# Kernel tuning notes

Measured on AMD Instinct MI355X. Metric: run time of the kernel, lower is better.

## Reference

```python
import jax, jax.numpy as jnp
import numpy as np

B_, S, D_IN, D_OUT, R = 4, 2048, 2048, 2048, 16

def setup_inputs() -> dict:
    key = jax.random.key(0)
    k = jax.random.split(key, 5)
    x = jax.random.normal(k[0], (B_, S, D_IN), dtype=jnp.float32)
    W = jax.random.normal(k[1], (D_OUT, D_IN), dtype=jnp.float32) * (1.0 / np.sqrt(D_IN))
    b = jax.random.normal(k[2], (D_OUT,), dtype=jnp.float32) * 0.02
    A = jax.random.normal(k[3], (R, D_IN), dtype=jnp.float32) * 0.02  # nn.init.normal_(std=0.02)
    Bm = jax.random.normal(k[4], (D_OUT, R), dtype=jnp.float32) * 0.02
    scale = jnp.asarray(0.8, dtype=jnp.float32)
    return {"x": x, "W": W, "b": b, "A": A, "B": Bm, "scale": scale}

def reference(x, W, b, A, B, scale):
    # base linear: y = x @ W^T + b
    orig = jnp.einsum('bsd,od->bso', x, W) + b
    # LoRA: scale * (x @ A^T) @ B^T
    h = jnp.einsum('bsd,rd->bsr', x, A)          # [B,S,r]
    lora = jnp.einsum('bsr,or->bso', h, B) * scale
    return orig + lora
```

## Files before the change

### kernel.cpp

```cpp
#include <hip/hip_runtime.h>
#include <hip/hip_bf16.h>
#include <cstdint>


typedef __bf16 bf16x8 __attribute__((ext_vector_type(8)));
typedef float floatx4 __attribute__((ext_vector_type(4)));
typedef unsigned short ushort8 __attribute__((ext_vector_type(8)));

#define BM 256
#define BN 256
#define BK 64

__device__ __forceinline__ void gload_lds16(const void* g, void* l) {
    __builtin_amdgcn_global_load_lds((__attribute__((address_space(1))) void*)g,
                                     (__attribute__((address_space(3))) void*)l,
                                     16, 0, 0);
}

__device__ __forceinline__ unsigned short f2bf_bits(float f) {
    unsigned int u = __float_as_uint(f);
    u += 0x7FFFu + ((u >> 16) & 1u);
    return (unsigned short)(u >> 16);
}

__global__ __launch_bounds__(256)
void aux_kernel(const float* __restrict__ x, unsigned short* __restrict__ Xbf,
                const float* __restrict__ W, const float* __restrict__ A,
                const float* __restrict__ Bm, const float* __restrict__ scale_p,
                unsigned short* __restrict__ Weff)
{
    const int K = 2048, R = 16;
    int bid = blockIdx.x;
    if (bid < 8192) {
        size_t i = ((size_t)bid * 256 + threadIdx.x) * 8;
        float4 a = *reinterpret_cast<const float4*>(x + i);
        float4 b = *reinterpret_cast<const float4*>(x + i + 4);
        ushort8 o;
        o[0] = f2bf_bits(a.x); o[1] = f2bf_bits(a.y);
        o[2] = f2bf_bits(a.z); o[3] = f2bf_bits(a.w);
        o[4] = f2bf_bits(b.x); o[5] = f2bf_bits(b.y);
        o[6] = f2bf_bits(b.z); o[7] = f2bf_bits(b.w);
        *reinterpret_cast<ushort8*>(Xbf + i) = o;
    } else {
        int t  = (bid - 8192) * 256 + threadIdx.x;
        int n  = t >> 8;
        int k8 = (t & 255) << 3;

        float s = *scale_p;
        float br[16];
#pragma unroll
        for (int r = 0; r < R; ++r)
            br[r] = s * Bm[n * R + r];

        float acc[8] = {0,0,0,0,0,0,0,0};
#pragma unroll
        for (int r = 0; r < R; ++r) {
            const float* ap = A + r * K + k8;
#pragma unroll
            for (int j = 0; j < 8; ++j)
                acc[j] += br[r] * ap[j];
        }

        const float* wp = W + (size_t)n * K + k8;
        ushort8 o;
#pragma unroll
        for (int j = 0; j < 8; ++j)
            o[j] = f2bf_bits(wp[j] + acc[j]);
        *reinterpret_cast<ushort8*>(Weff + (size_t)n * K + k8) = o;
    }
}

#define BAR()       __builtin_amdgcn_s_barrier()
#define WAIT_LGKM() asm volatile("s_waitcnt lgkmcnt(0)" ::: "memory")
#define WAIT_VM8()  asm volatile("s_waitcnt vmcnt(8)" ::: "memory")

#define STAGE(Ldst, Gsrc, koff) do {                                          \
    gload_lds16((Gsrc) + (koff),                   (Ldst) + tid * 8);         \
    gload_lds16((Gsrc) + (size_t)128 * K + (koff), (Ldst) + 4096 + tid * 8);  \
} while (0)

#define READ_A(buf, ks)                                                       \
    _Pragma("unroll")                                                         \
    for (int mi = 0; mi < 8; ++mi)                                            \
        af[mi] = *reinterpret_cast<const bf16x8*>(                            \
            &Sa[buf][ks][(arow + mi * 16) * 32 + aswz]);

#define READ_B(buf, ks, nh)                                                   \
    _Pragma("unroll")                                                         \
    for (int ni = 0; ni < 2; ++ni)                                            \
        bf[ni] = *reinterpret_cast<const bf16x8*>(                            \
            &Sb[buf][ks][(brow + (nh) * 32 + ni * 16) * 32 + aswz]);

#define MFMA_HALF(nh) do {                                                    \
    __builtin_amdgcn_s_setprio(1);                                            \
    _Pragma("unroll")                                                         \
    for (int mi = 0; mi < 8; ++mi) {                                          \
        acc[mi][(nh)*2+0] = __builtin_amdgcn_mfma_f32_16x16x32_bf16(          \
            af[mi], bf[0], acc[mi][(nh)*2+0], 0, 0, 0);                       \
        acc[mi][(nh)*2+1] = __builtin_amdgcn_mfma_f32_16x16x32_bf16(          \
            af[mi], bf[1], acc[mi][(nh)*2+1], 0, 0, 0);                       \
    }                                                                         \
    __builtin_amdgcn_s_setprio(0);                                            \
} while (0)

#define TILE(buf, kA, kB) do {                                                \
                                                       \
    READ_A(buf, 0); READ_B(buf, 0, 0);                                        \
    STAGE(&Sa[1-(buf)][1][0], gA, (kA));                                      \
    BAR(); WAIT_LGKM(); MFMA_HALF(0); BAR();                                  \
                                                       \
    READ_B(buf, 0, 1);                                                        \
    STAGE(&Sb[1-(buf)][1][0], gB, (kA));                                      \
    BAR(); WAIT_LGKM(); MFMA_HALF(1); WAIT_VM8(); BAR();                      \
                                                       \
    READ_A(buf, 1); READ_B(buf, 1, 0);                                        \
    STAGE(&Sa[buf][0][0], gA, (kB));                                          \
    BAR(); WAIT_LGKM(); MFMA_HALF(0); BAR();                                  \
                                                       \
    READ_B(buf, 1, 1);                                                        \
    STAGE(&Sb[buf][0][0], gB, (kB));                                          \
    BAR(); WAIT_LGKM(); MFMA_HALF(1); WAIT_VM8(); BAR();                      \
} while (0)

__global__ __launch_bounds__(512)
void gemm_bias_kernel(const unsigned short* __restrict__ X,
                      const unsigned short* __restrict__ Wt,
                      const float* __restrict__ bias,
                      float* __restrict__ out)
{
    const int N = 2048, K = 2048, NT = 32;

    __shared__ alignas(16) unsigned short Sa[2][2][256 * 32];
    __shared__ alignas(16) unsigned short Sb[2][2][256 * 32];

    const int tid  = threadIdx.x;
    const int wave = tid >> 6;
    const int lane = tid & 63;
    const int lrow = lane & 15;
    const int quad = lane >> 4;
    const int wr   = wave >> 2;
    const int wc   = wave & 3;

    const int id  = blockIdx.x;
    const int xcd = id & 7;
    const int sg  = id >> 3;
    const int bm  = (xcd * 4 + (sg & 3)) * BM;
    const int bn  = (sg >> 2) * BN;

    const int srow  = tid >> 2;
    const int sslot = tid & 3;
    const int sgcol = (sslot ^ ((srow >> 1) & 3)) << 3;
    const unsigned short* gA = X  + (size_t)(bm + srow) * K + sgcol;
    const unsigned short* gB = Wt + (size_t)(bn + srow) * K + sgcol;

    floatx4 acc[8][4] = {};
    bf16x8 af[8], bf[2];

    const int aswz = (quad ^ ((lrow >> 1) & 3)) << 3;
    const int arow = wr * 128 + lrow;
    const int brow = wc * 64 + lrow;

    STAGE(&Sa[0][0][0], gA, 0);
    STAGE(&Sb[0][0][0], gB, 0);
    STAGE(&Sa[0][1][0], gA, 32);
    STAGE(&Sb[0][1][0], gB, 32);
    STAGE(&Sa[1][0][0], gA, 64);
    STAGE(&Sb[1][0][0], gB, 64);
    WAIT_VM8(); BAR();

#pragma unroll 1
    for (int tt = 0; tt < NT; tt += 2) {
        const int ka0 = (tt + 1 < NT ? tt + 1 : NT - 1) * BK + 32;
        const int kb0 = (tt + 2 < NT ? tt + 2 : NT - 1) * BK;
        const int ka1 = (tt + 2 < NT ? tt + 2 : NT - 1) * BK + 32;
        const int kb1 = (tt + 3 < NT ? tt + 3 : NT - 1) * BK;
        TILE(0, ka0, kb0);
        TILE(1, ka1, kb1);
    }
    asm volatile("s_waitcnt vmcnt(0)" ::: "memory");

    float bsv[4];
#pragma unroll
    for (int ni = 0; ni < 4; ++ni)
        bsv[ni] = bias[bn + wc * 64 + ni * 16 + lrow];

    const int rbase = quad << 2;
#pragma unroll
    for (int mi = 0; mi < 8; ++mi) {
#pragma unroll
        for (int r = 0; r < 4; ++r) {
            size_t rowoff = (size_t)(bm + wr * 128 + mi * 16 + rbase + r) * N;
#pragma unroll
            for (int ni = 0; ni < 4; ++ni)
                out[rowoff + bn + wc * 64 + ni * 16 + lrow] = acc[mi][ni][r] + bsv[ni];
        }
    }
}

extern "C" void kernel_launch(void* const* d_in, const int* in_sizes, int n_in,
                              void* d_out, int out_size, void* d_ws, size_t ws_size,
                              hipStream_t stream)
{
    const float* x  = (const float*)d_in[0];
    const float* W  = (const float*)d_in[1];
    const float* b  = (const float*)d_in[2];
    const float* A  = (const float*)d_in[3];
    const float* Bm = (const float*)d_in[4];
    const float* sc = (const float*)d_in[5];
    float* out = (float*)d_out;

    const size_t M = 8192, N = 2048, K = 2048;

    unsigned short* Xbf  = (unsigned short*)d_ws;
    unsigned short* Weff = (unsigned short*)d_ws + M * K;

    aux_kernel<<<dim3((M * K + N * K) / 8 / 256), dim3(256), 0, stream>>>(
        x, Xbf, W, A, Bm, sc, Weff);

    gemm_bias_kernel<<<dim3((M / BM) * (N / BN)), dim3(512), 0, stream>>>(
        Xbf, Weff, b, out);
}
```

Measured before the change: 211.5 us.

## Restructure GEMM pipeline into quadrant stages with full-BK tiles and new swizzle

```diff
diff --git a/kernel.cpp b/kernel.cpp
--- a/kernel.cpp
+++ b/kernel.cpp
@@ -10,6 +10,7 @@
 #define BM 256
 #define BN 256
 #define BK 64
+#define NT 32
 
 __device__ __forceinline__ void gload_lds16(const void* g, void* l) {
     __builtin_amdgcn_global_load_lds((__attribute__((address_space(1))) void*)g,
@@ -72,54 +73,49 @@
 
 #define BAR()       __builtin_amdgcn_s_barrier()
 #define WAIT_LGKM() asm volatile("s_waitcnt lgkmcnt(0)" ::: "memory")
-#define WAIT_VM8()  asm volatile("s_waitcnt vmcnt(8)" ::: "memory")
-
-#define STAGE(Ldst, Gsrc, koff) do {                                          \
-    gload_lds16((Gsrc) + (koff),                   (Ldst) + tid * 8);         \
-    gload_lds16((Gsrc) + (size_t)128 * K + (koff), (Ldst) + 4096 + tid * 8);  \
-} while (0)
-
-#define READ_A(buf, ks)                                                       \
+#define WAIT_VM4()  asm volatile("s_waitcnt vmcnt(4)" ::: "memory")
+#define WAIT_VM0()  asm volatile("s_waitcnt vmcnt(0)" ::: "memory")
+
+#define STAGE_A(buf, mh, kt) do {                                             \
+    gload_lds16(gA0 + (size_t)(mh) * 64 * K + (kt) * 64, &Sa[buf][mh][c0 * 8]); \
+    gload_lds16(gA1 + (size_t)(mh) * 64 * K + (kt) * 64, &Sa[buf][mh][c1 * 8]); \
+} while (0)
+
+#define STAGE_B(buf, nh, kt) do {                                             \
+    gload_lds16(gB0 + (size_t)(nh) * 32 * K + (kt) * 64, &Sb[buf][nh][c0 * 8]); \
+    gload_lds16(gB1 + (size_t)(nh) * 32 * K + (kt) * 64, &Sb[buf][nh][c1 * 8]); \
+} while (0)
+
+#define READ_A(buf, mh) do {                                                  \
+    const unsigned short* ra = &Sa[buf][mh][(wr * 64 + lrow) * 64];           \
     _Pragma("unroll")                                                         \
-    for (int mi = 0; mi < 8; ++mi)                                            \
-        af[mi] = *reinterpret_cast<const bf16x8*>(                            \
-            &Sa[buf][ks][(arow + mi * 16) * 32 + aswz]);
-
-#define READ_B(buf, ks, nh)                                                   \
+    for (int mq = 0; mq < 4; ++mq) {                                          \
+        af[0][mq] = *reinterpret_cast<const bf16x8*>(ra + mq * 1024 + swz0);  \
+        af[1][mq] = *reinterpret_cast<const bf16x8*>(ra + mq * 1024 + swz1);  \
+    }                                                                         \
+} while (0)
+
+#define READ_B(buf, nh) do {                                                  \
+    const unsigned short* rb = &Sb[buf][nh][(wc * 32 + lrow) * 64];           \
     _Pragma("unroll")                                                         \
-    for (int ni = 0; ni < 2; ++ni)                                            \
-        bf[ni] = *reinterpret_cast<const bf16x8*>(                            \
-            &Sb[buf][ks][(brow + (nh) * 32 + ni * 16) * 32 + aswz]);
-
-#define MFMA_HALF(nh) do {                                                    \
+    for (int nq = 0; nq < 2; ++nq) {                                          \
+        bq[0][nq] = *reinterpret_cast<const bf16x8*>(rb + nq * 1024 + swz0);  \
+        bq[1][nq] = *reinterpret_cast<const bf16x8*>(rb + nq * 1024 + swz1);  \
+    }                                                                         \
+} while (0)
+
+#define MFMAQ(mh, nh) do {                                                    \
     __builtin_amdgcn_s_setprio(1);                                            \
     _Pragma("unroll")                                                         \
-    for (int mi = 0; mi < 8; ++mi) {                                          \
-        acc[mi][(nh)*2+0] = __builtin_amdgcn_mfma_f32_16x16x32_bf16(          \
-            af[mi], bf[0], acc[mi][(nh)*2+0], 0, 0, 0);                       \
-        acc[mi][(nh)*2+1] = __builtin_amdgcn_mfma_f32_16x16x32_bf16(          \
-            af[mi], bf[1], acc[mi][(nh)*2+1], 0, 0, 0);                       \
-    }                                                                         \
+    for (int mq = 0; mq < 4; ++mq)                                            \
+        _Pragma("unroll")                                                     \
+        for (int nq = 0; nq < 2; ++nq) {                                      \
+            floatx4 tmp = __builtin_amdgcn_mfma_f32_16x16x32_bf16(            \
+                af[0][mq], bq[0][nq], acc[(mh)*4+mq][(nh)*2+nq], 0, 0, 0);    \
+            acc[(mh)*4+mq][(nh)*2+nq] = __builtin_amdgcn_mfma_f32_16x16x32_bf16( \
+                af[1][mq], bq[1][nq], tmp, 0, 0, 0);                          \
+        }                                                                     \
     __builtin_amdgcn_s_setprio(0);                                            \
-} while (0)
-
-#define TILE(buf, kA, kB) do {                                                \
-                                                       \
-    READ_A(buf, 0); READ_B(buf, 0, 0);                                        \
-    STAGE(&Sa[1-(buf)][1][0], gA, (kA));                                      \
-    BAR(); WAIT_LGKM(); MFMA_HALF(0); BAR();                                  \
-                                                       \
-    READ_B(buf, 0, 1);                                                        \
-    STAGE(&Sb[1-(buf)][1][0], gB, (kA));                                      \
-    BAR(); WAIT_LGKM(); MFMA_HALF(1); WAIT_VM8(); BAR();                      \
-                                                       \
-    READ_A(buf, 1); READ_B(buf, 1, 0);                                        \
-    STAGE(&Sa[buf][0][0], gA, (kB));                                          \
-    BAR(); WAIT_LGKM(); MFMA_HALF(0); BAR();                                  \
-                                                       \
-    READ_B(buf, 1, 1);                                                        \
-    STAGE(&Sb[buf][0][0], gB, (kB));                                          \
-    BAR(); WAIT_LGKM(); MFMA_HALF(1); WAIT_VM8(); BAR();                      \
 } while (0)
 
 __global__ __launch_bounds__(512)
@@ -128,10 +124,10 @@
                       const float* __restrict__ bias,
                       float* __restrict__ out)
 {
-    const int N = 2048, K = 2048, NT = 32;
-
-    __shared__ alignas(16) unsigned short Sa[2][2][256 * 32];
-    __shared__ alignas(16) unsigned short Sb[2][2][256 * 32];
+    const int N = 2048, K = 2048;
+
+    __shared__ alignas(16) unsigned short Sa[2][2][8192];
+    __shared__ alignas(16) unsigned short Sb[2][2][8192];
 
     const int tid  = threadIdx.x;
     const int wave = tid >> 6;
@@ -147,52 +143,84 @@
     const int bm  = (xcd * 4 + (sg & 3)) * BM;
     const int bn  = (sg >> 2) * BN;
 
-    const int srow  = tid >> 2;
-    const int sslot = tid & 3;
-    const int sgcol = (sslot ^ ((srow >> 1) & 3)) << 3;
-    const unsigned short* gA = X  + (size_t)(bm + srow) * K + sgcol;
-    const unsigned short* gB = Wt + (size_t)(bn + srow) * K + sgcol;
+    const int c0 = tid, c1 = tid + 512;
+    const int ar0 = (c0 >> 3) & 63, as0 = c0 & 7;
+    const int ar1 = (c1 >> 3) & 63, as1 = c1 & 7;
+    const unsigned short* gA0 = X + (size_t)(bm + (c0 >> 9) * 128 + ar0) * K
+                                  + ((as0 ^ (ar0 & 7)) << 3);
+    const unsigned short* gA1 = X + (size_t)(bm + (c1 >> 9) * 128 + ar1) * K
+                                  + ((as1 ^ (ar1 & 7)) << 3);
+    const int br0 = (c0 >> 3) & 31, br1 = (c1 >> 3) & 31;
+    const unsigned short* gB0 = Wt + (size_t)(bn + (c0 >> 8) * 64 + br0) * K
+                                   + ((as0 ^ (br0 & 7)) << 3);
+    const unsigned short* gB1 = Wt + (size_t)(bn + (c1 >> 8) * 64 + br1) * K
+                                   + ((as1 ^ (br1 & 7)) << 3);
+
+    const int swz0 = (quad ^ (lrow & 7)) << 3;
+    const int swz1 = swz0 ^ 32;
 
     floatx4 acc[8][4] = {};
-    bf16x8 af[8], bf[2];
-
-    const int aswz = (quad ^ ((lrow >> 1) & 3)) << 3;
-    const int arow = wr * 128 + lrow;
-    const int brow = wc * 64 + lrow;
-
-    STAGE(&Sa[0][0][0], gA, 0);
-    STAGE(&Sb[0][0][0], gB, 0);
-    STAGE(&Sa[0][1][0], gA, 32);
-    STAGE(&Sb[0][1][0], gB, 32);
-    STAGE(&Sa[1][0][0], gA, 64);
-    STAGE(&Sb[1][0][0], gB, 64);
-    WAIT_VM8(); BAR();
+    bf16x8 af[2][4];
+    bf16x8 bq[2][2];
+
+    STAGE_A(0, 0, 0);
+    STAGE_B(0, 1, 0);
+    STAGE_B(0, 0, 0);
+    STAGE_A(0, 1, 0);
+    STAGE_A(1, 0, 1);
+    STAGE_B(1, 1, 1);
+    WAIT_VM4(); BAR();
 
 #pragma unroll 1
     for (int tt = 0; tt < NT; tt += 2) {
-        const int ka0 = (tt + 1 < NT ? tt + 1 : NT - 1) * BK + 32;
-        const int kb0 = (tt + 2 < NT ? tt + 2 : NT - 1) * BK;
-        const int ka1 = (tt + 2 < NT ? tt + 2 : NT - 1) * BK + 32;
-        const int kb1 = (tt + 3 < NT ? tt + 3 : NT - 1) * BK;
-        TILE(0, ka0, kb0);
-        TILE(1, ka1, kb1);
+        const int t1 = tt + 1;
+        const int t2 = (tt + 2 < NT) ? tt + 2 : NT - 1;
+        const int t3 = (tt + 3 < NT) ? tt + 3 : NT - 1;
+
+        READ_A(0, 0); READ_B(0, 0);
+        STAGE_B(1, 0, t1);
+        BAR(); WAIT_LGKM(); MFMAQ(0, 0); BAR();
+        READ_B(0, 1);
+        STAGE_A(1, 1, t1);
+        BAR(); WAIT_LGKM(); MFMAQ(0, 1); BAR();
+        READ_A(0, 1);
+        STAGE_A(0, 0, t2);
+        BAR(); WAIT_LGKM(); MFMAQ(1, 1); BAR();
+        READ_B(0, 0);
+        STAGE_B(0, 1, t2);
+        BAR(); WAIT_LGKM(); MFMAQ(1, 0); WAIT_VM4(); BAR();
+
+        READ_A(1, 0); READ_B(1, 0);
+        STAGE_B(0, 0, t2);
+        BAR(); WAIT_LGKM(); MFMAQ(0, 0); BAR();
+        READ_B(1, 1);
+        STAGE_A(0, 1, t2);
+        BAR(); WAIT_LGKM(); MFMAQ(0, 1); BAR();
+        READ_A(1, 1);
+        STAGE_A(1, 0, t3);
+        BAR(); WAIT_LGKM(); MFMAQ(1, 1); BAR();
+        READ_B(1, 0);
+        STAGE_B(1, 1, t3);
+        BAR(); WAIT_LGKM(); MFMAQ(1, 0); WAIT_VM4(); BAR();
     }
-    asm volatile("s_waitcnt vmcnt(0)" ::: "memory");
+    WAIT_VM0();
 
     float bsv[4];
 #pragma unroll
     for (int ni = 0; ni < 4; ++ni)
-        bsv[ni] = bias[bn + wc * 64 + ni * 16 + lrow];
+        bsv[ni] = bias[bn + wc * 64 + (ni >> 1) * 32 + (ni & 1) * 16 + lrow];
 
     const int rbase = quad << 2;
 #pragma unroll
     for (int mi = 0; mi < 8; ++mi) {
 #pragma unroll
         for (int r = 0; r < 4; ++r) {
-            size_t rowoff = (size_t)(bm + wr * 128 + mi * 16 + rbase + r) * N;
+            size_t rowoff = (size_t)(bm + wr * 128 + (mi >> 2) * 64
+                                     + (mi & 3) * 16 + rbase + r) * N;
 #pragma unroll
             for (int ni = 0; ni < 4; ++ni)
-                out[rowoff + bn + wc * 64 + ni * 16 + lrow] = acc[mi][ni][r] + bsv[ni];
+                out[rowoff + bn + wc * 64 + (ni >> 1) * 32 + (ni & 1) * 16 + lrow]
+                    = acc[mi][ni][r] + bsv[ni];
         }
     }
 }
```

Measured after the change: 207.5 us. About the same (-1.9%).
